# Optimization experiments

Hardware: AMD Instinct MI355X
Metric: run time of the kernel (lower is better)

The kernel has to match this reference:

```python
import jax, jax.numpy as jnp
import numpy as np

DIM = 128        # per-head dim == model width in this module
Q_HEADS = 16
KV_HEADS = 4
WINDOW = 512
BATCH = 4
SEQ = 2048


def setup_inputs() -> dict:
    key = jax.random.key(0)
    k1, k2, k3 = jax.random.split(key, 3)
    x = jax.random.normal(k1, (BATCH, SEQ, DIM), dtype=jnp.float32)
    # fused qkv weight, stored (in, out) so forward is x @ W_qkv
    W_qkv = jax.random.normal(k2, (DIM, (Q_HEADS + 2 * KV_HEADS) * DIM), dtype=jnp.float32) * (DIM ** -0.5)
    W_proj = jax.random.normal(k3, (Q_HEADS * DIM, DIM), dtype=jnp.float32) * ((Q_HEADS * DIM) ** -0.5)
    return {"x": x, "W_qkv": W_qkv, "W_proj": W_proj}


def _gqa_forward(x, W_qkv, W_proj):
    b, s, d = x.shape
    qkv = x @ W_qkv                                    # [b, s, (Hq+2Hkv)*d]
    qkv = qkv.reshape(b, s, Q_HEADS + 2 * KV_HEADS, d).transpose(0, 2, 1, 3)
    q = qkv[:, :Q_HEADS]                               # [b, Hq, s, d]
    k = qkv[:, Q_HEADS:Q_HEADS + KV_HEADS]             # [b, Hkv, s, d]
    v = qkv[:, Q_HEADS + KV_HEADS:]                    # [b, Hkv, s, d]

    # GQA: repeat kv heads to match q heads
    group = Q_HEADS // KV_HEADS
    k = jnp.repeat(k, group, axis=1)                   # [b, Hq, s, d]
    v = jnp.repeat(v, group, axis=1)

    scale = 1.0 / jnp.sqrt(jnp.float32(d))
    scores = jnp.einsum('bhqd,bhkd->bhqk', q, k) * scale   # [b, Hq, s, s]

    q_idx = jnp.arange(s)[:, None]
    kv_idx = jnp.arange(s)[None, :]
    rel = (q_idx - kv_idx).astype(jnp.float32)         # [s, s]
    # per-head ALiBi slope: exp2(-(h+1)*8/Hq), added (sign matches source)
    h = jnp.arange(Q_HEADS, dtype=jnp.float32)
    slopes = jnp.exp2(-((h + 1.0) * 8.0 / Q_HEADS))    # [Hq]
    scores = scores + slopes[None, :, None, None] * rel[None, None, :, :]

    mask = (q_idx >= kv_idx) & ((q_idx - kv_idx) <= WINDOW)
    scores = jnp.where(mask[None, None], scores, -jnp.inf)
    probs = jax.nn.softmax(scores, axis=-1)

    att = jnp.einsum('bhqk,bhkd->bhqd', probs, v)      # [b, Hq, s, d]
    att = att.transpose(0, 2, 1, 3).reshape(b, s, Q_HEADS * d)
    return att @ W_proj                                # [b, s, d]


def reference(x, W_qkv, W_proj):
    return _gqa_forward(x, W_qkv, W_proj)
```

## Files before the change

kernel.cpp:

```cpp
#include <hip/hip_runtime.h>
#include <math.h>

#define DIM_    128
#define QH_     16
#define KVH_    4
#define WIN_    512
#define BATCH_  4
#define SEQ_    2048
#define QKV_LD  3072

#define QB_LD   3136
#define VG_LD   2112
#define AH_LD   2112
#define WP_LD   2112

#define NX   (BATCH_*SEQ_*DIM_)
#define NWQ  (DIM_*QKV_LD)

typedef __attribute__((ext_vector_type(8))) short short8;
typedef __attribute__((ext_vector_type(4))) float f32x4;
typedef unsigned short u16;
typedef unsigned int u32;

__device__ __forceinline__ u16 f2bf(float f) {
    u32 u = __float_as_uint(f);
    u += 0x7fff + ((u >> 16) & 1);
    return (u16)(u >> 16);
}
__device__ __forceinline__ float bf2f(u16 u) {
    return __uint_as_float(((u32)u) << 16);
}
__device__ __forceinline__ u32 pkbf(float a, float b) {
    u32 r;
    __asm__("v_cvt_pk_bf16_f32 %0, %1, %2" : "=v"(r) : "v"(a), "v"(b));
    return r;
}
#define MFMA16 __builtin_amdgcn_mfma_f32_16x16x32_bf16

#if __has_builtin(__builtin_amdgcn_exp2f)
#define EXP2F __builtin_amdgcn_exp2f
#else
#define EXP2F exp2f
#endif

__device__ __forceinline__ void gload_lds16(const u16* g, u16* l) {
    __builtin_amdgcn_global_load_lds(
        (const __attribute__((address_space(1))) unsigned int*)(const void*)g,
        (__attribute__((address_space(3))) unsigned int*)(void*)l, 16, 0, 0);
}

__global__ __launch_bounds__(256) void prep(
    const float* __restrict__ x, const float* __restrict__ Wqkv,
    const float* __restrict__ Wproj,
    u16* __restrict__ xh, u16* __restrict__ wth, u16* __restrict__ wpth)
{
    if (blockIdx.x < 1024) {
        const size_t t = (size_t)blockIdx.x * 256 + threadIdx.x;
        float4 v = *(const float4*)(x + 4 * t);
        ushort4 o;
        o.x = f2bf(v.x); o.y = f2bf(v.y); o.z = f2bf(v.z); o.w = f2bf(v.w);
        *(ushort4*)(xh + 4 * t) = o;
        return;
    }
    __shared__ float T[32][33];
    int tile = blockIdx.x - 1024;
    const float* src; u16* dst; int N, ldo;
    if (tile < 384) { src = Wqkv;  dst = wth;  N = 3072; ldo = 128; }
    else { tile -= 384; src = Wproj; dst = wpth; N = 128; ldo = WP_LD; }
    const int ntile = N >> 5;
    const int k0 = (tile / ntile) << 5, n0 = (tile % ntile) << 5;
    const int tx = threadIdx.x & 31, ty = threadIdx.x >> 5;
    #pragma unroll
    for (int i = 0; i < 4; ++i)
        T[ty + 8 * i][tx] = src[(size_t)(k0 + ty + 8 * i) * N + n0 + tx];
    __syncthreads();
    #pragma unroll
    for (int i = 0; i < 4; ++i)
        dst[(size_t)(n0 + ty + 8 * i) * ldo + k0 + tx] = f2bf(T[tx][ty + 8 * i]);
}

__global__ __launch_bounds__(256) void gemm1_mfma(
    const u16* __restrict__ xh, const u16* __restrict__ wth,
    u16* __restrict__ qkvb, u16* __restrict__ vg)
{
    const int bn = blockIdx.x * 256;
    const int mc = blockIdx.y * 128;
    const int tid = threadIdx.x;
    const int wv = tid >> 6, lane = tid & 63;
    const int lo = lane & 15, hi = lane >> 4;
    const int lr = lo, quad = hi;
    const int wn = bn + wv * 64;

    __shared__ u16 Ct[2][16][264];

    short8 bf[4][4];
    #pragma unroll
    for (int nt = 0; nt < 4; ++nt)
        #pragma unroll
        for (int s = 0; s < 4; ++s)
            bf[nt][s] = *(const short8*)(
                wth + (size_t)(wn + nt * 16 + lo) * DIM_ + s * 32 + hi * 8);

    const bool qk = (bn < 2560);
    const u16* aA = xh + (size_t)(mc + lo) * DIM_ + hi * 8;
    const int sr = tid >> 4, sc = tid & 15;

#define G1BODY(AF, IT) do {                                                   \
    f32x4 acc[4] = {};                                                        \
    if (qk) {                                                                 \
        _Pragma("unroll")                                                     \
        for (int s = 0; s < 4; ++s)                                           \
            _Pragma("unroll")                                                 \
            for (int nt = 0; nt < 4; ++nt)                                    \
                acc[nt] = MFMA16(bf[nt][s], AF[s], acc[nt], 0, 0, 0);         \
        const int bufq = (IT) & 1;                                            \
        _Pragma("unroll")                                                     \
        for (int nt = 0; nt < 4; ++nt) {                                      \
            uint2 o;                                                          \
            o.x = pkbf(acc[nt][0], acc[nt][1]);                               \
            o.y = pkbf(acc[nt][2], acc[nt][3]);                               \
            *(uint2*)&Ct[bufq][lr][wv * 64 + nt * 16 + quad * 4] = o;         \
        }                                                                     \
        __syncthreads();                                                      \
        const int row = mc + (IT) * 16 + sr;                                  \
        u16* drow = qkvb + (size_t)row * QB_LD + bn;                          \
        short8 v0 = *(const short8*)&Ct[bufq][sr][sc * 8];                    \
        short8 v1 = *(const short8*)&Ct[bufq][sr][128 + sc * 8];              \
        *(short8*)(drow + sc * 8) = v0;                                       \
        *(short8*)(drow + 128 + sc * 8) = v1;                                 \
    } else {                                                                  \
        _Pragma("unroll")                                                     \
        for (int s = 0; s < 4; ++s)                                           \
            _Pragma("unroll")                                                 \
            for (int nt = 0; nt < 4; ++nt)                                    \
                acc[nt] = MFMA16(AF[s], bf[nt][s], acc[nt], 0, 0, 0);         \
        const int m0 = mc + (IT) * 16 + quad * 4;                             \
        const int bb = m0 >> 11, mseq = m0 & 2047;                            \
        _Pragma("unroll")                                                     \
        for (int nt = 0; nt < 4; ++nt) {                                      \
            const int ncol = wn + nt * 16 + lr - 2560;                        \
            const int kvh = ncol >> 7, d = ncol & 127;                        \
            uint2 o;                                                          \
            o.x = pkbf(acc[nt][0], acc[nt][1]);                               \
            o.y = pkbf(acc[nt][2], acc[nt][3]);                               \
            *(uint2*)(vg + ((size_t)(bb * KVH_ + kvh) * DIM_ + d) * VG_LD     \
                      + mseq) = o;                                            \
        }                                                                     \
    }                                                                         \
} while (0)

    short8 afA[4], afB[4];
    #pragma unroll
    for (int s = 0; s < 4; ++s) afA[s] = *(const short8*)(aA + s * 32);

    #pragma unroll 1
    for (int it = 0; it < 8; it += 2) {
        const u16* aN = aA + (size_t)(it + 1) * 16 * DIM_;
        #pragma unroll
        for (int s = 0; s < 4; ++s) afB[s] = *(const short8*)(aN + s * 32);
        G1BODY(afA, it);
        const int nx = (it + 2 < 8) ? (it + 2) : 7;
        const u16* aN2 = aA + (size_t)nx * 16 * DIM_;
        #pragma unroll
        for (int s = 0; s < 4; ++s) afA[s] = *(const short8*)(aN2 + s * 32);
        G1BODY(afB, it + 1);
    }
#undef G1BODY
}

__global__ __launch_bounds__(512) void attn_mfma(
    const u16* __restrict__ qkvb, const u16* __restrict__ vg,
    u16* __restrict__ ah)
{
    const int xcd  = blockIdx.x & 7;
    const int idx  = blockIdx.x >> 3;
    const int pair = xcd + 8 * (idx & 1);
    const int qt   = idx >> 1;
    const int b    = pair >> 2, kvh = pair & 3;
    const int q0 = qt << 5;
    const int tid = threadIdx.x;
    const int wv8 = tid >> 6, lane = tid & 63;
    const int hq = wv8 >> 1, mrow = wv8 & 1;
    const int lr = lane & 15, quad = lane >> 4;
    const int h = kvh * 4 + hq;
    const bool oddq = (quad & 1) != 0;

    __shared__ u16 Kb[2][16][512];
    __shared__ u16 Vb[2][16][512];

    const float scale2 = 0.08838834764831845f * 1.4426950408889634f;
    const float slope2 = exp2f(-0.5f * (float)(h + 1)) * 1.4426950408889634f;
    const int jbase = max(0, q0 - WIN_);
    const int nch = (q0 + 32 - jbase + 63) >> 6;
    const size_t rowb = (size_t)b * SEQ_;
    const u16* kgp = qkvb + rowb * QB_LD + (QH_ + kvh) * DIM_;
    const u16* vgb = vg + (size_t)(b * KVH_ + kvh) * DIM_ * VG_LD;
    const int lo = lane & 15, hi = lane >> 4;

    short8 qf[4];
    {
        const u16* qp = qkvb + (rowb + q0 + mrow * 16 + lr) * QB_LD
                        + h * DIM_ + quad * 8;
        #pragma unroll
        for (int s = 0; s < 4; ++s) qf[s] = *(const short8*)(qp + 32 * s);
    }

    float alpha0;
    {
        const int q = q0 + mrow * 16 + lr;
        const int rm = (q < WIN_) ? q : WIN_;
        alpha0 = slope2 * (float)(q - rm);
    }

    f32x4 O[8] = {};
    float rs = 0.f;

    #define STAGE(CH, SLOT) do {                                              \
        const int _jk = jbase + ((CH) << 6);                                  \
        _Pragma("unroll")                                                     \
        for (int _t = 0; _t < 2; ++_t) {                                      \
            const int _p = wv8 + _t * 8;                                      \
            int _kr = _jk + (_p >> 2) * 16 + lo;                              \
            _kr = (_kr < SEQ_) ? _kr : (SEQ_ - 1);                            \
            gload_lds16(kgp + (size_t)_kr * QB_LD + (_p & 3) * 32 + hi * 8,   \
                        &Kb[(SLOT)][_p][0]);                                  \
            int _kc = _jk + (_p & 1) * 32 + hi * 8;                           \
            _kc = (_kc < SEQ_ - 8) ? _kc : (SEQ_ - 8);                        \
            gload_lds16(vgb + (size_t)((_p >> 1) * 16 + lo) * VG_LD + _kc,    \
                        &Vb[(SLOT)][_p][0]);                                  \
        }                                                                     \
    } while (0)

    STAGE(0, 0);

    for (int ch = 0; ch < nch; ++ch) {
        const int jk = jbase + (ch << 6);
        const int slot = ch & 1;
        __asm__ volatile("s_waitcnt vmcnt(0)" ::: "memory");
        __asm__ volatile("s_barrier" ::: "memory");
        if (ch + 1 < nch) STAGE(ch + 1, slot ^ 1);

        u32 pw[4][2];
        const int qm0 = q0 + mrow * 16;
        #pragma unroll
        for (int nt = 0; nt < 4; ++nt) {
            f32x4 c = {0.f, 0.f, 0.f, 0.f};
            __builtin_amdgcn_s_setprio(1);
            #pragma unroll
            for (int s = 0; s < 4; ++s) {
                short8 kf = *(const short8*)&Kb[slot][nt * 4 + s][lane * 8];
                c = MFMA16(kf, qf[s], c, 0, 0, 0);
            }
            __builtin_amdgcn_s_setprio(0);
            const int jknt = jk + nt * 16;
            const float b0 = fmaf(-slope2, (float)(jknt + quad * 4), alpha0);
            float e0, e1, e2, e3;
            if (qm0 >= jknt + 15 && qm0 + 15 <= jknt + WIN_) {
                e0 = EXP2F(fmaf(c[0], scale2, b0));
                e1 = EXP2F(fmaf(c[1], scale2, b0 - slope2));
                e2 = EXP2F(fmaf(c[2], scale2, b0 - 2.f * slope2));
                e3 = EXP2F(fmaf(c[3], scale2, b0 - 3.f * slope2));
            } else {
                const int q = qm0 + lr, j0q = jknt + quad * 4;
                float ee[4];
                #pragma unroll
                for (int r = 0; r < 4; ++r) {
                    const int rel = q - (j0q + r);
                    const float t = fmaf(c[r], scale2, b0 - (float)r * slope2);
                    ee[r] = ((unsigned)rel <= (unsigned)WIN_) ? EXP2F(t) : 0.f;
                }
                e0 = ee[0]; e1 = ee[1]; e2 = ee[2]; e3 = ee[3];
            }
            rs += (e0 + e1) + (e2 + e3);
            pw[nt][0] = pkbf(e0, e1);
            pw[nt][1] = pkbf(e2, e3);
        }

        short8 pa[2];
        #pragma unroll
        for (int g = 0; g < 2; ++g) {
            union { u32 w[4]; short8 s; } P;
            #pragma unroll
            for (int w = 0; w < 2; ++w) {
                auto r = __builtin_amdgcn_permlane32_swap(
                    pw[2 * g][w], pw[2 * g + 1][w], false, false);
                const u32 rx = r[0], ry = r[1];
                const u32 sx = (u32)__shfl_xor((int)rx, 16);
                const u32 sy = (u32)__shfl_xor((int)ry, 16);
                P.w[w]     = oddq ? sy : rx;
                P.w[2 + w] = oddq ? ry : sx;
            }
            pa[g] = P.s;
        }

        __builtin_amdgcn_s_setprio(1);
        #pragma unroll
        for (int nt = 0; nt < 8; ++nt) {
            short8 vf0 = *(const short8*)&Vb[slot][nt * 2][lane * 8];
            short8 vf1 = *(const short8*)&Vb[slot][nt * 2 + 1][lane * 8];
            O[nt] = MFMA16(vf0, pa[0], O[nt], 0, 0, 0);
            O[nt] = MFMA16(vf1, pa[1], O[nt], 0, 0, 0);
        }
        __builtin_amdgcn_s_setprio(0);
    }
    #undef STAGE

    __asm__ volatile("s_waitcnt vmcnt(0)" ::: "memory");

    rs += __shfl_xor(rs, 16);
    rs += __shfl_xor(rs, 32);

    {
        const float inv = 1.0f / rs;
        u16* dst = ah + (rowb + q0 + mrow * 16 + lr) * (size_t)AH_LD
                   + h * DIM_;
        #pragma unroll
        for (int nt = 0; nt < 8; ++nt) {
            uint2 o;
            o.x = pkbf(O[nt][0] * inv, O[nt][1] * inv);
            o.y = pkbf(O[nt][2] * inv, O[nt][3] * inv);
            *(uint2*)(dst + nt * 16 + quad * 4) = o;
        }
    }
}

__global__ __launch_bounds__(512) void gemm2_mfma(
    const u16* __restrict__ ah, const u16* __restrict__ wpth,
    float* __restrict__ out)
{
    const int bm = blockIdx.x * 32;
    const int tid = threadIdx.x;
    const int wv8 = tid >> 6, lane = tid & 63;
    const int wr = wv8 >> 2, wc = wv8 & 3;
    const int lr = lane & 15, quad = lane >> 4;

    __shared__ u16 At2[2][32][520];

    #define G2STAGE(KS, SLOT) do {                                            \
        _Pragma("unroll")                                                     \
        for (int _t = 0; _t < 4; ++_t) {                                      \
            const int _r = wv8 * 4 + _t;                                      \
            gload_lds16(ah + (size_t)(bm + _r) * AH_LD + (KS) * 512           \
                        + lane * 8, &At2[(SLOT)][_r][0]);                     \
        }                                                                     \
    } while (0)

    f32x4 acc[2] = {};

    G2STAGE(0, 0);

    #pragma unroll 1
    for (int ks = 0; ks < 4; ++ks) {
        const int slot = ks & 1;
        __asm__ volatile("s_waitcnt vmcnt(0)" ::: "memory");
        __asm__ volatile("s_barrier" ::: "memory");
        if (ks < 3) G2STAGE(ks + 1, slot ^ 1);

        const u16* wbase = wpth + (size_t)(wc * 32 + lr) * WP_LD
                           + ks * 512 + quad * 8;
        #pragma unroll
        for (int s = 0; s < 16; ++s) {
            short8 wf0 = *(const short8*)(wbase + s * 32);
            short8 wf1 = *(const short8*)(wbase + (size_t)16 * WP_LD + s * 32);
            short8 af  = *(const short8*)
                &At2[slot][wr * 16 + lr][s * 32 + quad * 8];
            acc[0] = MFMA16(wf0, af, acc[0], 0, 0, 0);
            acc[1] = MFMA16(wf1, af, acc[1], 0, 0, 0);
        }
    }
    #undef G2STAGE

    __asm__ volatile("s_waitcnt vmcnt(0)" ::: "memory");

    #pragma unroll
    for (int nt = 0; nt < 2; ++nt) {
        float* orow = out + (size_t)(bm + wr * 16 + lr) * DIM_
                      + wc * 32 + nt * 16 + quad * 4;
        *(float4*)orow = *(float4*)&acc[nt];
    }
}

extern "C" void kernel_launch(void* const* d_in, const int* in_sizes, int n_in,
                              void* d_out, int out_size, void* d_ws, size_t ws_size,
                              hipStream_t stream)
{
    const float* x     = (const float*)d_in[0];
    const float* Wqkv  = (const float*)d_in[1];
    const float* Wproj = (const float*)d_in[2];
    float* out = (float*)d_out;

    u16* xh   = (u16*)d_ws;
    u16* wth  = xh   + (size_t)NX;
    u16* wpth = wth  + (size_t)NWQ;
    u16* qkvb = wpth + (size_t)DIM_ * WP_LD;
    u16* vg   = qkvb + (size_t)8192 * QB_LD;
    u16* ahp  = vg   + (size_t)BATCH_ * KVH_ * DIM_ * VG_LD;

    prep<<<1024 + 640, 256, 0, stream>>>(x, Wqkv, Wproj, xh, wth, wpth);

    gemm1_mfma<<<dim3(12, 64), 256, 0, stream>>>(xh, wth, qkvb, vg);

    attn_mfma<<<1024, 512, 0, stream>>>(qkvb, vg, ahp);

    gemm2_mfma<<<8192 / 32, 512, 0, stream>>>(ahp, wpth, out);
}
```

Measured before the change: 179.3 us.

## Interleave softmax exp with PV MFMAs and batch QK MFMAs across tiles

Reorders the per-chunk attention loop. The four QK^T accumulator tiles are now computed in an interleaved s-outer loop, so consecutive MFMAs are independent. The exp/pack work for later key sub-tiles is then interleaved with the PV MFMAs for the first half of P, aiming to overlap VALU/transcendental work with matrix-core work. The s_setprio hints are removed. In exchange it uses more live registers (four accumulators at once), which may affect occupancy, and leaves the overlap to the compiler's instruction scheduling.

New measurement: 209.6 us. +16.9%, slower.

```diff
diff --git a/kernel.cpp b/kernel.cpp
--- a/kernel.cpp
+++ b/kernel.cpp
@@ -231,6 +231,47 @@
         }                                                                     \
     } while (0)
 
+    #define SM(NT) do {                                                       \
+        const int jknt = jk + (NT) * 16;                                      \
+        const float b0 = fmaf(-slope2, (float)(jknt + quad * 4), alpha0);     \
+        float e0, e1, e2, e3;                                                 \
+        if (qm0 >= jknt + 15 && qm0 + 15 <= jknt + WIN_) {                    \
+            e0 = EXP2F(fmaf(c[NT][0], scale2, b0));                           \
+            e1 = EXP2F(fmaf(c[NT][1], scale2, b0 - slope2));                  \
+            e2 = EXP2F(fmaf(c[NT][2], scale2, b0 - 2.f * slope2));            \
+            e3 = EXP2F(fmaf(c[NT][3], scale2, b0 - 3.f * slope2));            \
+        } else {                                                              \
+            const int q = qm0 + lr, j0q = jknt + quad * 4;                    \
+            float ee[4];                                                      \
+            _Pragma("unroll")                                                 \
+            for (int r = 0; r < 4; ++r) {                                     \
+                const int rel = q - (j0q + r);                                \
+                const float t = fmaf(c[NT][r], scale2,                        \
+                                     b0 - (float)r * slope2);                 \
+                ee[r] = ((unsigned)rel <= (unsigned)WIN_) ? EXP2F(t) : 0.f;   \
+            }                                                                 \
+            e0 = ee[0]; e1 = ee[1]; e2 = ee[2]; e3 = ee[3];                   \
+        }                                                                     \
+        rs += (e0 + e1) + (e2 + e3);                                          \
+        pw[NT][0] = pkbf(e0, e1);                                             \
+        pw[NT][1] = pkbf(e2, e3);                                             \
+    } while (0)
+
+    #define REDIST(G, PA) do {                                                \
+        union { u32 w[4]; short8 s; } P;                                      \
+        _Pragma("unroll")                                                     \
+        for (int w = 0; w < 2; ++w) {                                         \
+            auto r = __builtin_amdgcn_permlane32_swap(                        \
+                pw[2 * (G)][w], pw[2 * (G) + 1][w], false, false);            \
+            const u32 rx = r[0], ry = r[1];                                   \
+            const u32 sx = (u32)__shfl_xor((int)rx, 16);                      \
+            const u32 sy = (u32)__shfl_xor((int)ry, 16);                      \
+            P.w[w]     = oddq ? sy : rx;                                      \
+            P.w[2 + w] = oddq ? ry : sx;                                      \
+        }                                                                     \
+        PA = P.s;                                                             \
+    } while (0)
+
     STAGE(0, 0);
 
     for (int ch = 0; ch < nch; ++ch) {
@@ -240,70 +281,44 @@
         __asm__ volatile("s_barrier" ::: "memory");
         if (ch + 1 < nch) STAGE(ch + 1, slot ^ 1);
 
+        const int qm0 = q0 + mrow * 16;
         u32 pw[4][2];
-        const int qm0 = q0 + mrow * 16;
+
+        f32x4 c[4] = {};
+        #pragma unroll
+        for (int s = 0; s < 4; ++s)
+            #pragma unroll
+            for (int nt = 0; nt < 4; ++nt) {
+                short8 kf = *(const short8*)&Kb[slot][nt * 4 + s][lane * 8];
+                c[nt] = MFMA16(kf, qf[s], c[nt], 0, 0, 0);
+            }
+
+        short8 pa0, pa1;
+        SM(0);
+        SM(1);
+        REDIST(0, pa0);
+        SM(2);
         #pragma unroll
         for (int nt = 0; nt < 4; ++nt) {
-            f32x4 c = {0.f, 0.f, 0.f, 0.f};
-            __builtin_amdgcn_s_setprio(1);
-            #pragma unroll
-            for (int s = 0; s < 4; ++s) {
-                short8 kf = *(const short8*)&Kb[slot][nt * 4 + s][lane * 8];
-                c = MFMA16(kf, qf[s], c, 0, 0, 0);
-            }
-            __builtin_amdgcn_s_setprio(0);
-            const int jknt = jk + nt * 16;
-            const float b0 = fmaf(-slope2, (float)(jknt + quad * 4), alpha0);
-            float e0, e1, e2, e3;
-            if (qm0 >= jknt + 15 && qm0 + 15 <= jknt + WIN_) {
-                e0 = EXP2F(fmaf(c[0], scale2, b0));
-                e1 = EXP2F(fmaf(c[1], scale2, b0 - slope2));
-                e2 = EXP2F(fmaf(c[2], scale2, b0 - 2.f * slope2));
-                e3 = EXP2F(fmaf(c[3], scale2, b0 - 3.f * slope2));
-            } else {
-                const int q = qm0 + lr, j0q = jknt + quad * 4;
-                float ee[4];
-                #pragma unroll
-                for (int r = 0; r < 4; ++r) {
-                    const int rel = q - (j0q + r);
-                    const float t = fmaf(c[r], scale2, b0 - (float)r * slope2);
-                    ee[r] = ((unsigned)rel <= (unsigned)WIN_) ? EXP2F(t) : 0.f;
-                }
-                e0 = ee[0]; e1 = ee[1]; e2 = ee[2]; e3 = ee[3];
-            }
-            rs += (e0 + e1) + (e2 + e3);
-            pw[nt][0] = pkbf(e0, e1);
-            pw[nt][1] = pkbf(e2, e3);
+            short8 vf = *(const short8*)&Vb[slot][nt * 2][lane * 8];
+            O[nt] = MFMA16(vf, pa0, O[nt], 0, 0, 0);
         }
-
-        short8 pa[2];
-        #pragma unroll
-        for (int g = 0; g < 2; ++g) {
-            union { u32 w[4]; short8 s; } P;
-            #pragma unroll
-            for (int w = 0; w < 2; ++w) {
-                auto r = __builtin_amdgcn_permlane32_swap(
-                    pw[2 * g][w], pw[2 * g + 1][w], false, false);
-                const u32 rx = r[0], ry = r[1];
-                const u32 sx = (u32)__shfl_xor((int)rx, 16);
-                const u32 sy = (u32)__shfl_xor((int)ry, 16);
-                P.w[w]     = oddq ? sy : rx;
-                P.w[2 + w] = oddq ? ry : sx;
-            }
-            pa[g] = P.s;
+        SM(3);
+        #pragma unroll
+        for (int nt = 4; nt < 8; ++nt) {
+            short8 vf = *(const short8*)&Vb[slot][nt * 2][lane * 8];
+            O[nt] = MFMA16(vf, pa0, O[nt], 0, 0, 0);
         }
-
-        __builtin_amdgcn_s_setprio(1);
+        REDIST(1, pa1);
         #pragma unroll
         for (int nt = 0; nt < 8; ++nt) {
-            short8 vf0 = *(const short8*)&Vb[slot][nt * 2][lane * 8];
-            short8 vf1 = *(const short8*)&Vb[slot][nt * 2 + 1][lane * 8];
-            O[nt] = MFMA16(vf0, pa[0], O[nt], 0, 0, 0);
-            O[nt] = MFMA16(vf1, pa[1], O[nt], 0, 0, 0);
+            short8 vf = *(const short8*)&Vb[slot][nt * 2 + 1][lane * 8];
+            O[nt] = MFMA16(vf, pa1, O[nt], 0, 0, 0);
         }
-        __builtin_amdgcn_s_setprio(0);
     }
     #undef STAGE
+    #undef SM
+    #undef REDIST
 
     __asm__ volatile("s_waitcnt vmcnt(0)" ::: "memory");
 
```
